# Kernel optimization log

Measured on AMD Instinct MI355X. Metric: run time of the kernel, lower is better.

Reference implementation:

```python
import jax, jax.numpy as jnp
import numpy as np

D_MODEL = 1024
N_HEADS = 16
D_K = D_MODEL // N_HEADS
D_FF = 4096
EPS = 1e-5


def _layer_norm(x, gamma, beta):
    mu = jnp.mean(x, axis=-1, keepdims=True)
    var = jnp.var(x, axis=-1, keepdims=True)
    return (x - mu) * jax.lax.rsqrt(var + EPS) * gamma + beta


def setup_inputs() -> dict:
    key = jax.random.key(0)
    ks = jax.random.split(key, 16)
    s = 1.0 / np.sqrt(D_MODEL)
    sf = 1.0 / np.sqrt(D_FF)
    return {
        "x": jax.random.normal(ks[0], (2, 2048, D_MODEL), dtype=jnp.float32),
        "Wq": jax.random.uniform(ks[1], (D_MODEL, D_MODEL), minval=-s, maxval=s),
        "bq": jax.random.uniform(ks[2], (D_MODEL,), minval=-s, maxval=s),
        "Wk": jax.random.uniform(ks[3], (D_MODEL, D_MODEL), minval=-s, maxval=s),
        "bk": jax.random.uniform(ks[4], (D_MODEL,), minval=-s, maxval=s),
        "Wv": jax.random.uniform(ks[5], (D_MODEL, D_MODEL), minval=-s, maxval=s),
        "bv": jax.random.uniform(ks[6], (D_MODEL,), minval=-s, maxval=s),
        "Wo": jax.random.uniform(ks[7], (D_MODEL, D_MODEL), minval=-s, maxval=s),
        "bo": jax.random.uniform(ks[8], (D_MODEL,), minval=-s, maxval=s),
        "W1": jax.random.uniform(ks[9], (D_MODEL, D_FF), minval=-s, maxval=s),
        "b1": jax.random.uniform(ks[10], (D_FF,), minval=-s, maxval=s),
        "W2": jax.random.uniform(ks[11], (D_FF, D_MODEL), minval=-sf, maxval=sf),
        "b2": jax.random.uniform(ks[12], (D_MODEL,), minval=-sf, maxval=sf),
        "g1": jnp.ones((D_MODEL,)),
        "be1": jnp.zeros((D_MODEL,)),
        "g2": jnp.ones((D_MODEL,)),
        "be2": jnp.zeros((D_MODEL,)),
    }


def reference(x, Wq, bq, Wk, bk, Wv, bv, Wo, bo, W1, b1, W2, b2, g1, be1, g2, be2):
    B, S, _ = x.shape

    def heads(y):  # (B,S,D) -> (B,H,S,dk)
        return y.reshape(B, S, N_HEADS, D_K).transpose(0, 2, 1, 3)

    q = heads(x @ Wq + bq)
    k = heads(x @ Wk + bk)
    v = heads(x @ Wv + bv)

    scores = jnp.einsum("bhqd,bhkd->bhqk", q, k) / np.sqrt(D_K)
    attn = jax.nn.softmax(scores, axis=-1)
    out = jnp.einsum("bhqk,bhkd->bhqd", attn, v)
    out = out.transpose(0, 2, 1, 3).reshape(B, S, D_MODEL)
    attn_out = out @ Wo + bo

    resid_mid = _layer_norm(x + attn_out, g1, be1)
    ff = jnp.maximum(resid_mid @ W1 + b1, 0.0) @ W2 + b2
    return _layer_norm(resid_mid + ff, g2, be2)
```

## Files before the change

kernel.cpp:

```cpp
#include <hip/hip_runtime.h>

#define DM   1024
#define DFF  4096
#define NH   16
#define DKH  64
#define SEQ  2048
#define BATCH 2
#define ROWS (BATCH*SEQ)
#define QKS  2048

typedef __bf16 bf16x8 __attribute__((ext_vector_type(8)));
typedef float  f32x4  __attribute__((ext_vector_type(4)));

__device__ __forceinline__ unsigned short f2b(float f) {
    unsigned int u = __builtin_bit_cast(unsigned int, f);
    u += 0x7fffu + ((u >> 16) & 1u);
    return (unsigned short)(u >> 16);
}
__device__ __forceinline__ float b2f(unsigned short u) {
    return __builtin_bit_cast(float, (unsigned int)u << 16);
}
__device__ __forceinline__ float exp2_raw(float x) {
    float r;
    asm("v_exp_f32 %0, %1" : "=v"(r) : "v"(x));
    return r;
}

__device__ __forceinline__ void gl_lds16(const unsigned short* g, unsigned short* l) {
    __builtin_amdgcn_global_load_lds(
        (const __attribute__((address_space(1))) unsigned int*)(const void*)g,
        (__attribute__((address_space(3))) unsigned int*)(void*)l, 16, 0, 0);
}

__global__ __launch_bounds__(256) void k_prep(const float* __restrict__ x,
                                              const float* __restrict__ Wq,
                                              const float* __restrict__ Wk,
                                              const float* __restrict__ Wv,
                                              const float* __restrict__ Wo,
                                              const float* __restrict__ W1,
                                              const float* __restrict__ W2,
                                              unsigned short* __restrict__ xb,
                                              unsigned short* __restrict__ WqkT,
                                              unsigned short* __restrict__ WvT,
                                              unsigned short* __restrict__ WoT,
                                              unsigned short* __restrict__ W1T,
                                              unsigned short* __restrict__ W2T) {
    int z = blockIdx.z;
    int bid = blockIdx.y * gridDim.x + blockIdx.x;
    int tx = threadIdx.x, ty = threadIdx.y;
    if (z == 6) {
        int i = bid * 256 + ty * 32 + tx;
        float4 v = ((const float4*)x)[i];
        ushort4 u;
        u.x = f2b(v.x); u.y = f2b(v.y); u.z = f2b(v.z); u.w = f2b(v.w);
        ((ushort4*)xb)[i] = u;
        return;
    }
    const float* W; unsigned short* WT; int R, C;
    if      (z == 0) { W = Wq; WT = WqkT;                     R = DM;  C = DM;  }
    else if (z == 1) { W = Wk; WT = WqkT + (size_t)DM * DM;   R = DM;  C = DM;  }
    else if (z == 2) { W = Wv; WT = WvT;                      R = DM;  C = DM;  }
    else if (z == 3) { W = Wo; WT = WoT;                      R = DM;  C = DM;  }
    else if (z == 4) { W = W1; WT = W1T;                      R = DM;  C = DFF; }
    else             { W = W2; WT = W2T;                      R = DFF; C = DM;  }
    int ct = C / 32;
    if (bid >= (R / 32) * ct) return;
    int c0 = (bid % ct) * 32, r0 = (bid / ct) * 32;
    __shared__ float t[32][33];
#pragma unroll
    for (int i = 0; i < 4; i++) {
        int r = ty + i * 8;
        t[r][tx] = W[(size_t)(r0 + r) * C + c0 + tx];
    }
    __syncthreads();
#pragma unroll
    for (int i = 0; i < 4; i++) {
        int r = ty + i * 8;
        WT[(size_t)(c0 + r) * R + r0 + tx] = f2b(t[tx][r]);
    }
}

template<int WM, int WN, bool OUTF32, bool RELU, bool BIASROW, bool VPERM, bool SCALE2, bool SPLITK, bool SUPER2D>
__global__ __launch_bounds__(256) void k_gemm_bt(const unsigned short* __restrict__ A,
                                                 const unsigned short* __restrict__ BT,
                                                 const float* __restrict__ bias,
                                                 const float* __restrict__ bias2,
                                                 int bsplit, float sc2,
                                                 void* __restrict__ Cout,
                                                 int M, int N, int K) {
    constexpr int BM = 2 * WM, BN = 2 * WN;
    constexpr int MT = WM / 16, NT = WN / 16;
    constexpr int IA = BM / 32, IB = BN / 32;
    __shared__ unsigned short As[BM][64] __attribute__((aligned(16)));
    __shared__ unsigned short Bs[BN][64] __attribute__((aligned(16)));
    int tid = threadIdx.x;
    int w = tid >> 6, l = tid & 63;
    int wr = w >> 1, wc = w & 1;
    int l15 = l & 15, lg = l >> 4;

    int bid = blockIdx.y * gridDim.x + blockIdx.x;
    int nwg = gridDim.x * gridDim.y;
    int m0, n0;
    if (SUPER2D) {
        int xcd = bid & 7, q = bid >> 3;
        int RM = gridDim.y >> 1, RN = gridDim.x >> 2;
        int mI = (xcd >> 2) * RM + (q % RM);
        int nI = (xcd & 3) * RN + (q / RM);
        m0 = mI * BM; n0 = nI * BN;
    } else {
        int swz = (bid & 7) * (nwg >> 3) + (bid >> 3);
        m0 = (swz / gridDim.x) * BM; n0 = (swz % gridDim.x) * BN;
    }

    int kb_ = SPLITK ? (int)blockIdx.z * (K >> 1) : 0;
    int Keff = SPLITK ? (K >> 1) : K;

    int lr8 = l >> 3;
    int gsrc = (l & 7) ^ lr8;
    const unsigned short* Abase = A  + (size_t)(m0 + w * (BM / 4) + lr8) * K + kb_ + gsrc * 8;
    const unsigned short* Bbase = BT + (size_t)(n0 + w * (BN / 4) + lr8) * K + kb_ + gsrc * 8;

    f32x4 acc[MT][NT] = {};

    int nk = Keff >> 6;
    for (int kt = 0; kt < nk; ++kt) {
        __syncthreads();
#pragma unroll
        for (int it = 0; it < IA; ++it)
            gl_lds16(Abase + (size_t)(it * 8) * K + kt * 64, &As[w * (BM / 4) + it * 8][0]);
#pragma unroll
        for (int it = 0; it < IB; ++it)
            gl_lds16(Bbase + (size_t)(it * 8) * K + kt * 64, &Bs[w * (BN / 4) + it * 8][0]);
        __syncthreads();
#pragma unroll
        for (int ks = 0; ks < 2; ++ks) {
            int glog = ks * 4 + lg;
            bf16x8 af[MT], bfr[NT];
#pragma unroll
            for (int mt = 0; mt < MT; ++mt) {
                int row = wr * WM + mt * 16 + l15;
                af[mt] = *(const bf16x8*)&As[row][(glog ^ (row & 7)) << 3];
            }
#pragma unroll
            for (int nt = 0; nt < NT; ++nt) {
                int row = wc * WN + nt * 16 + l15;
                bfr[nt] = *(const bf16x8*)&Bs[row][(glog ^ (row & 7)) << 3];
            }
#pragma unroll
            for (int mt = 0; mt < MT; ++mt)
#pragma unroll
                for (int nt = 0; nt < NT; ++nt)
                    acc[mt][nt] = __builtin_amdgcn_mfma_f32_16x16x32_bf16(af[mt], bfr[nt], acc[mt][nt], 0, 0, 0);
        }
    }
    float*          CoutF = (float*)Cout          + (SPLITK ? (size_t)blockIdx.z * M * N : 0);
    unsigned short* CoutH = (unsigned short*)Cout + (SPLITK ? (size_t)blockIdx.z * M * N : 0);
    float browv[MT][4];
    if (BIASROW) {
#pragma unroll
        for (int mt = 0; mt < MT; ++mt)
#pragma unroll
            for (int r = 0; r < 4; ++r)
                browv[mt][r] = bias[m0 + wr * WM + mt * 16 + lg * 4 + r];
    }
#pragma unroll
    for (int nt = 0; nt < NT; ++nt) {
        int colo = VPERM ? (32 * (nt >> 1) + 4 * (nt & 1) + 8 * (l15 >> 2) + (l15 & 3))
                         : (nt * 16 + l15);
        int col = n0 + wc * WN + colo;
        float bv = BIASROW ? 0.f : (col < bsplit ? bias[col] : bias2[col - bsplit]);
        if (SPLITK && blockIdx.z != 0) bv = 0.f;
#pragma unroll
        for (int mt = 0; mt < MT; ++mt) {
#pragma unroll
            for (int r = 0; r < 4; ++r) {
                int row = m0 + wr * WM + mt * 16 + lg * 4 + r;
                float v = acc[mt][nt][r] + (BIASROW ? browv[mt][r] : bv);
                if (SCALE2 && col >= bsplit) v *= sc2;
                if (RELU) v = fmaxf(v, 0.f);
                if (OUTF32) CoutF[(size_t)row * N + col] = v;
                else        CoutH[(size_t)row * N + col] = f2b(v);
            }
        }
    }
}

__global__ __launch_bounds__(256) void k_gemm_qkv(const unsigned short* __restrict__ xb,
                                                  const unsigned short* __restrict__ WqkT,
                                                  const unsigned short* __restrict__ WvT,
                                                  const float* __restrict__ bq,
                                                  const float* __restrict__ bk,
                                                  const float* __restrict__ bv,
                                                  float sc,
                                                  unsigned short* __restrict__ qkb,
                                                  unsigned short* __restrict__ vT) {
    constexpr int BM = 64, BN = 128, MT = 2, NT = 4, IA = 2, IB = 4;
    const int K = DM;
    __shared__ unsigned short As[BM][64] __attribute__((aligned(16)));
    __shared__ unsigned short Bs[BN][64] __attribute__((aligned(16)));
    int tid = threadIdx.x;
    int w = tid >> 6, l = tid & 63;
    int wr = w >> 1, wc = w & 1;
    int l15 = l & 15, lg = l >> 4;

    int bid1 = blockIdx.x;
    bool isQK = bid1 < 1024;
    const unsigned short *A, *BT;
    int m0, n0;
    if (isQK) {
        int bid = bid1;
        int swz = (bid & 7) * 128 + (bid >> 3);
        m0 = (swz / 16) * BM; n0 = (swz % 16) * BN;
        A = xb; BT = WqkT;
    } else {
        int bid = bid1 - 1024;
        int swz = (bid & 7) * 64 + (bid >> 3);
        m0 = (swz / 32) * BM; n0 = (swz % 32) * BN;
        A = WvT; BT = xb;
    }

    int lr8 = l >> 3;
    int gsrc = (l & 7) ^ lr8;
    const unsigned short* Abase = A  + (size_t)(m0 + w * (BM / 4) + lr8) * K + gsrc * 8;
    const unsigned short* Bbase = BT + (size_t)(n0 + w * (BN / 4) + lr8) * K + gsrc * 8;

    f32x4 acc[MT][NT] = {};

    for (int kt = 0; kt < K / 64; ++kt) {
        __syncthreads();
#pragma unroll
        for (int it = 0; it < IA; ++it)
            gl_lds16(Abase + (size_t)(it * 8) * K + kt * 64, &As[w * (BM / 4) + it * 8][0]);
#pragma unroll
        for (int it = 0; it < IB; ++it)
            gl_lds16(Bbase + (size_t)(it * 8) * K + kt * 64, &Bs[w * (BN / 4) + it * 8][0]);
        __syncthreads();
#pragma unroll
        for (int ks = 0; ks < 2; ++ks) {
            int glog = ks * 4 + lg;
            bf16x8 af[MT], bfr[NT];
#pragma unroll
            for (int mt = 0; mt < MT; ++mt) {
                int row = wr * 32 + mt * 16 + l15;
                af[mt] = *(const bf16x8*)&As[row][(glog ^ (row & 7)) << 3];
            }
#pragma unroll
            for (int nt = 0; nt < NT; ++nt) {
                int row = wc * 64 + nt * 16 + l15;
                bfr[nt] = *(const bf16x8*)&Bs[row][(glog ^ (row & 7)) << 3];
            }
#pragma unroll
            for (int mt = 0; mt < MT; ++mt)
#pragma unroll
                for (int nt = 0; nt < NT; ++nt)
                    acc[mt][nt] = __builtin_amdgcn_mfma_f32_16x16x32_bf16(af[mt], bfr[nt], acc[mt][nt], 0, 0, 0);
        }
    }

    if (isQK) {
#pragma unroll
        for (int nt = 0; nt < NT; ++nt) {
            int col = n0 + wc * 64 + nt * 16 + l15;
            float bvx = col < DM ? bq[col] : bk[col - DM];
#pragma unroll
            for (int mt = 0; mt < MT; ++mt)
#pragma unroll
                for (int r = 0; r < 4; ++r) {
                    int row = m0 + wr * 32 + mt * 16 + lg * 4 + r;
                    float v = acc[mt][nt][r] + bvx;
                    if (col >= DM) v *= sc;
                    qkb[(size_t)row * QKS + col] = f2b(v);
                }
        }
    } else {
        float browv[MT][4];
#pragma unroll
        for (int mt = 0; mt < MT; ++mt)
#pragma unroll
            for (int r = 0; r < 4; ++r)
                browv[mt][r] = bv[m0 + wr * 32 + mt * 16 + lg * 4 + r];
#pragma unroll
        for (int nt = 0; nt < NT; ++nt) {
            int colo = 32 * (nt >> 1) + 4 * (nt & 1) + 8 * (l15 >> 2) + (l15 & 3);
            int col = n0 + wc * 64 + colo;
#pragma unroll
            for (int mt = 0; mt < MT; ++mt)
#pragma unroll
                for (int r = 0; r < 4; ++r) {
                    int row = m0 + wr * 32 + mt * 16 + lg * 4 + r;
                    vT[(size_t)row * ROWS + col] = f2b(acc[mt][nt][r] + browv[mt][r]);
                }
        }
    }
}

__global__ __launch_bounds__(512) void k_attn(const unsigned short* __restrict__ Q,
                                              const unsigned short* __restrict__ Kb,
                                              const unsigned short* __restrict__ VT,
                                              unsigned short* __restrict__ O) {
    __shared__ unsigned short ks[2][128][64] __attribute__((aligned(16)));
    __shared__ unsigned short vs[2][2][64][64] __attribute__((aligned(16)));

    int tid = threadIdx.x;
    int w = tid >> 6, l = tid & 63;
    int l15 = l & 15, lg = l >> 4;

    int bid = blockIdx.y * gridDim.x + blockIdx.x;
    int bh = (bid & 7) * 4 + ((bid >> 3) & 3);
    int qt = bid >> 5;
    int b = bh >> 4, h = bh & 15;
    int row0 = qt * 128;

    const unsigned short* qg  = Q  + (size_t)b * SEQ * QKS + h * DKH;
    const unsigned short* kg  = Kb + (size_t)b * SEQ * QKS + h * DKH;
    const unsigned short* vtg = VT + (size_t)(h * DKH) * ROWS + (size_t)b * SEQ;

    int lr8 = l >> 3;
    int gsrc = (l & 7) ^ lr8;

    const unsigned short* kp = kg  + (size_t)(w * 16 + lr8) * QKS + gsrc * 8;
    const unsigned short* vp = vtg + (size_t)(w * 8 + lr8) * ROWS + gsrc * 8;

    gl_lds16(kp,                  &ks[0][w * 16][0]);
    gl_lds16(kp + (size_t)8 * QKS, &ks[0][w * 16 + 8][0]);
    gl_lds16(vp,                  &vs[0][0][w * 8][0]);
    gl_lds16(vp + 64,             &vs[0][1][w * 8][0]);
    kp += (size_t)128 * QKS; vp += 128;

    bf16x8 aq[2];
    {
        int qrow = row0 + w * 16 + l15;
        aq[0] = *(const bf16x8*)(qg + (size_t)qrow * QKS + lg * 8);
        aq[1] = *(const bf16x8*)(qg + (size_t)qrow * QKS + (4 + lg) * 8);
    }

    int dsoff[2][4];
#pragma unroll
    for (int ksi = 0; ksi < 2; ksi++)
#pragma unroll
        for (int nt = 0; nt < 4; nt++) {
            int row = nt * 16 + l15;
            int glog = ksi * 4 + lg;
            dsoff[ksi][nt] = row * 128 + ((glog ^ (row & 7)) << 4);
        }

    union { bf16x8 v; unsigned int u[4]; } ones;
#pragma unroll
    for (int i = 0; i < 4; i++) ones.u[i] = 0x3f803f80u;

    f32x4 o[4] = {};
    f32x4 osum = {};

    __syncthreads();

    int cur = 0;
    for (int kt = 0; kt < SEQ / 128; ++kt) {
        if (kt + 1 < SEQ / 128) {
            gl_lds16(kp,                   &ks[cur ^ 1][w * 16][0]);
            gl_lds16(kp + (size_t)8 * QKS, &ks[cur ^ 1][w * 16 + 8][0]);
            gl_lds16(vp,                   &vs[cur ^ 1][0][w * 8][0]);
            gl_lds16(vp + 64,              &vs[cur ^ 1][1][w * 8][0]);
            kp += (size_t)128 * QKS; vp += 128;
        }

#pragma unroll
        for (int hf = 0; hf < 2; ++hf) {
            const char* kbase = (const char*)&ks[cur][hf * 64][0];
            const char* vbase = (const char*)&vs[cur][hf][0][0];

            f32x4 s[4] = {};
            __builtin_amdgcn_s_setprio(1);
#pragma unroll
            for (int ksi = 0; ksi < 2; ksi++)
#pragma unroll
                for (int nt = 0; nt < 4; nt++) {
                    bf16x8 bk = *(const bf16x8*)(kbase + dsoff[ksi][nt]);
                    s[nt] = __builtin_amdgcn_mfma_f32_16x16x32_bf16(bk, aq[ksi], s[nt], 0, 0, 0);
                }
            __builtin_amdgcn_s_setprio(0);

            union { bf16x8 v; unsigned int u[4]; } A0, A1;
#pragma unroll
            for (int nt = 0; nt < 4; nt++)
#pragma unroll
                for (int w2 = 0; w2 < 2; w2++) {
                    float e0 = exp2_raw(s[nt][2 * w2]);
                    float e1 = exp2_raw(s[nt][2 * w2 + 1]);
                    unsigned int pk;
                    asm("v_cvt_pk_bf16_f32 %0, %1, %2" : "=v"(pk) : "v"(e0), "v"(e1));
                    if (nt < 2) A0.u[(nt & 1) * 2 + w2] = pk;
                    else        A1.u[(nt & 1) * 2 + w2] = pk;
                }

            __builtin_amdgcn_s_setprio(1);
            osum = __builtin_amdgcn_mfma_f32_16x16x32_bf16(A0.v, ones.v, osum, 0, 0, 0);
            osum = __builtin_amdgcn_mfma_f32_16x16x32_bf16(A1.v, ones.v, osum, 0, 0, 0);
#pragma unroll
            for (int ksi = 0; ksi < 2; ksi++)
#pragma unroll
                for (int nt = 0; nt < 4; nt++) {
                    bf16x8 bv = *(const bf16x8*)(vbase + dsoff[ksi][nt]);
                    o[nt] = __builtin_amdgcn_mfma_f32_16x16x32_bf16(ksi == 0 ? A0.v : A1.v, bv, o[nt], 0, 0, 0);
                }
            __builtin_amdgcn_s_setprio(0);
        }

        __syncthreads();
        cur ^= 1;
    }

    float rinv[4];
#pragma unroll
    for (int r = 0; r < 4; r++) rinv[r] = 1.f / osum[r];

    unsigned short* og = O + (size_t)b * SEQ * DM + h * DKH;
#pragma unroll
    for (int nt = 0; nt < 4; nt++) {
        int d = nt * 16 + l15;
#pragma unroll
        for (int r = 0; r < 4; r++) {
            int srow_ = row0 + w * 16 + lg * 4 + r;
            og[(size_t)srow_ * DM + d] = f2b(o[nt][r] * rinv[r]);
        }
    }
}

template<bool A16, bool WF32, bool WB16, bool ADD3, bool BC16>
__global__ __launch_bounds__(256) void k_add_ln(const void* __restrict__ a,
                                                const void* __restrict__ b,
                                                const void* __restrict__ c,
                                                const float* __restrict__ gamma,
                                                const float* __restrict__ beta,
                                                float* __restrict__ outf,
                                                unsigned short* __restrict__ outb) {
    __shared__ float red[8];
    int row = blockIdx.x, tid = threadIdx.x;
    float4 va;
    if (A16) {
        ushort4 ua = ((const ushort4*)((const unsigned short*)a + (size_t)row * DM))[tid];
        va.x = b2f(ua.x); va.y = b2f(ua.y); va.z = b2f(ua.z); va.w = b2f(ua.w);
    } else {
        va = ((const float4*)((const float*)a + (size_t)row * DM))[tid];
    }
    float4 vb, vc;
    if (BC16) {
        ushort4 ub = ((const ushort4*)((const unsigned short*)b + (size_t)row * DM))[tid];
        vb.x = b2f(ub.x); vb.y = b2f(ub.y); vb.z = b2f(ub.z); vb.w = b2f(ub.w);
    } else {
        vb = ((const float4*)((const float*)b + (size_t)row * DM))[tid];
    }
    float4 v;
    v.x = va.x + vb.x; v.y = va.y + vb.y; v.z = va.z + vb.z; v.w = va.w + vb.w;
    if (ADD3) {
        if (BC16) {
            ushort4 uc = ((const ushort4*)((const unsigned short*)c + (size_t)row * DM))[tid];
            vc.x = b2f(uc.x); vc.y = b2f(uc.y); vc.z = b2f(uc.z); vc.w = b2f(uc.w);
        } else {
            vc = ((const float4*)((const float*)c + (size_t)row * DM))[tid];
        }
        v.x += vc.x; v.y += vc.y; v.z += vc.z; v.w += vc.w;
    }
    float s = v.x + v.y + v.z + v.w;
    float q = v.x * v.x + v.y * v.y + v.z * v.z + v.w * v.w;
#pragma unroll
    for (int m = 1; m < 64; m <<= 1) { s += __shfl_xor(s, m); q += __shfl_xor(q, m); }
    if ((tid & 63) == 0) { red[tid >> 6] = s; red[4 + (tid >> 6)] = q; }
    __syncthreads();
    float tot  = red[0] + red[1] + red[2] + red[3];
    float totq = red[4] + red[5] + red[6] + red[7];
    float mu = tot * (1.f / DM);
    float var = totq * (1.f / DM) - mu * mu;
    float rs = rsqrtf(var + 1e-5f);
    float4 g  = ((const float4*)gamma)[tid];
    float4 be = ((const float4*)beta)[tid];
    float4 y;
    y.x = (v.x - mu) * rs * g.x + be.x;
    y.y = (v.y - mu) * rs * g.y + be.y;
    y.z = (v.z - mu) * rs * g.z + be.z;
    y.w = (v.w - mu) * rs * g.w + be.w;
    if (WF32) ((float4*)(outf + (size_t)row * DM))[tid] = y;
    if (WB16) {
        ushort4 u;
        u.x = f2b(y.x); u.y = f2b(y.y); u.z = f2b(y.z); u.w = f2b(y.w);
        ((ushort4*)(outb + (size_t)row * DM))[tid] = u;
    }
}

extern "C" void kernel_launch(void* const* d_in, const int* in_sizes, int n_in,
                              void* d_out, int out_size, void* d_ws, size_t ws_size,
                              hipStream_t stream) {
    const float* x   = (const float*)d_in[0];
    const float* Wq  = (const float*)d_in[1];
    const float* bq  = (const float*)d_in[2];
    const float* Wk  = (const float*)d_in[3];
    const float* bk  = (const float*)d_in[4];
    const float* Wv  = (const float*)d_in[5];
    const float* bv  = (const float*)d_in[6];
    const float* Wo  = (const float*)d_in[7];
    const float* bo  = (const float*)d_in[8];
    const float* W1  = (const float*)d_in[9];
    const float* b1  = (const float*)d_in[10];
    const float* W2  = (const float*)d_in[11];
    const float* b2  = (const float*)d_in[12];
    const float* g1  = (const float*)d_in[13];
    const float* be1 = (const float*)d_in[14];
    const float* g2  = (const float*)d_in[15];
    const float* be2 = (const float*)d_in[16];

    char* ws = (char*)d_ws;
    const size_t MB = 1u << 20;
    unsigned short* xb    = (unsigned short*)(ws + 0);
    unsigned short* WqkT  = (unsigned short*)(ws + 8 * MB);
    unsigned short* WvT   = (unsigned short*)(ws + 12 * MB);
    unsigned short* WoT   = (unsigned short*)(ws + 14 * MB);
    unsigned short* W1T   = (unsigned short*)(ws + 16 * MB);
    unsigned short* W2T   = (unsigned short*)(ws + 24 * MB);
    unsigned short* qkb   = (unsigned short*)(ws + 32 * MB);
    unsigned short* vT    = (unsigned short*)(ws + 48 * MB);
    unsigned short* prtb  = (unsigned short*)(ws + 32 * MB);
    unsigned short* residb= (unsigned short*)(ws + 88 * MB);
    unsigned short* h1    = (unsigned short*)(ws + 96 * MB);

    dim3 blk(256);
    const int BIG = 1 << 30;
    const float SC = 0.125f * 1.44269504f;

    k_prep<<<dim3(128, 32, 7), dim3(32, 8), 0, stream>>>(x, Wq, Wk, Wv, Wo, W1, W2,
                                                         xb, WqkT, WvT, WoT, W1T, W2T);

    k_gemm_qkv<<<dim3(1536), blk, 0, stream>>>(xb, WqkT, WvT, bq, bk, bv, SC, qkb, vT);

    k_attn<<<dim3(SEQ / 128, BATCH * NH), dim3(512), 0, stream>>>(qkb, qkb + DM, vT, xb);

    k_gemm_bt<32, 64, false, false, false, false, false, true, false><<<dim3(DM / 128, ROWS / 64, 2), blk, 0, stream>>>(
        xb, WoT, bo, bo, BIG, 1.f, prtb, ROWS, DM, DM);
    k_add_ln<false, false, true, true, true><<<ROWS, blk, 0, stream>>>(
        x, prtb, prtb + (size_t)ROWS * DM, g1, be1, nullptr, residb);

    k_gemm_bt<64, 64, false, true, false, false, false, false, true><<<dim3(DFF / 128, ROWS / 128), blk, 0, stream>>>(
        residb, W1T, b1, b1, BIG, 1.f, h1, ROWS, DFF, DM);
    k_gemm_bt<32, 64, false, false, false, false, false, true, false><<<dim3(DM / 128, ROWS / 64, 2), blk, 0, stream>>>(
        h1, W2T, b2, b2, BIG, 1.f, prtb, ROWS, DM, DFF);
    k_add_ln<true, true, false, true, true><<<ROWS, blk, 0, stream>>>(
        residb, prtb, prtb + (size_t)ROWS * DM, g2, be2, (float*)d_out, nullptr);
}
```

Measured before the change: 217.2 us.

## Split attention KV sequence across two wave groups and combine partials in LDS

The attention kernel now launches 1024 threads per block. Two groups of 8 waves each process half of the key/value sequence (1024 keys) for the same 128 query rows, using 64-key tiles with per-group double buffers. At the end, group 1 writes its unnormalized output and row sums to LDS, and group 0 adds them before normalizing and storing. The aim is more waves in flight per query tile to hide latency, at the cost of an extra barrier, an LDS reduction and higher register pressure from launch_bounds(1024, 8). This only works because the softmax uses no running max, so partial sums can be added directly.

```diff
diff --git a/kernel.cpp b/kernel.cpp
--- a/kernel.cpp
+++ b/kernel.cpp
@@ -294,15 +294,15 @@
     }
 }
 
-__global__ __launch_bounds__(512) void k_attn(const unsigned short* __restrict__ Q,
-                                              const unsigned short* __restrict__ Kb,
-                                              const unsigned short* __restrict__ VT,
-                                              unsigned short* __restrict__ O) {
-    __shared__ unsigned short ks[2][128][64] __attribute__((aligned(16)));
-    __shared__ unsigned short vs[2][2][64][64] __attribute__((aligned(16)));
+__global__ __launch_bounds__(1024, 8) void k_attn(const unsigned short* __restrict__ Q,
+                                                  const unsigned short* __restrict__ Kb,
+                                                  const unsigned short* __restrict__ VT,
+                                                  unsigned short* __restrict__ O) {
+    __shared__ unsigned short lds[32768] __attribute__((aligned(16)));
 
     int tid = threadIdx.x;
     int w = tid >> 6, l = tid & 63;
+    int wg = w >> 3, wl = w & 7;
     int l15 = l & 15, lg = l >> 4;
 
     int bid = blockIdx.y * gridDim.x + blockIdx.x;
@@ -318,18 +318,20 @@
     int lr8 = l >> 3;
     int gsrc = (l & 7) ^ lr8;
 
-    const unsigned short* kp = kg  + (size_t)(w * 16 + lr8) * QKS + gsrc * 8;
-    const unsigned short* vp = vtg + (size_t)(w * 8 + lr8) * ROWS + gsrc * 8;
-
-    gl_lds16(kp,                  &ks[0][w * 16][0]);
-    gl_lds16(kp + (size_t)8 * QKS, &ks[0][w * 16 + 8][0]);
-    gl_lds16(vp,                  &vs[0][0][w * 8][0]);
-    gl_lds16(vp + 64,             &vs[0][1][w * 8][0]);
-    kp += (size_t)128 * QKS; vp += 128;
+    unsigned short* kbuf[2] = { lds + (wg * 2 + 0) * 4096, lds + (wg * 2 + 1) * 4096 };
+    unsigned short* vbuf[2] = { lds + 16384 + (wg * 2 + 0) * 4096,
+                                lds + 16384 + (wg * 2 + 1) * 4096 };
+
+    const unsigned short* kp = kg  + (size_t)(wg * 1024 + wl * 8 + lr8) * QKS + gsrc * 8;
+    const unsigned short* vp = vtg + (size_t)(wl * 8 + lr8) * ROWS + wg * 1024 + gsrc * 8;
+
+    gl_lds16(kp, kbuf[0] + (wl * 8) * 64);
+    gl_lds16(vp, vbuf[0] + (wl * 8) * 64);
+    kp += (size_t)64 * QKS; vp += 64;
 
     bf16x8 aq[2];
     {
-        int qrow = row0 + w * 16 + l15;
+        int qrow = row0 + wl * 16 + l15;
         aq[0] = *(const bf16x8*)(qg + (size_t)qrow * QKS + lg * 8);
         aq[1] = *(const bf16x8*)(qg + (size_t)qrow * QKS + (4 + lg) * 8);
     }
@@ -354,73 +356,89 @@
     __syncthreads();
 
     int cur = 0;
-    for (int kt = 0; kt < SEQ / 128; ++kt) {
-        if (kt + 1 < SEQ / 128) {
-            gl_lds16(kp,                   &ks[cur ^ 1][w * 16][0]);
-            gl_lds16(kp + (size_t)8 * QKS, &ks[cur ^ 1][w * 16 + 8][0]);
-            gl_lds16(vp,                   &vs[cur ^ 1][0][w * 8][0]);
-            gl_lds16(vp + 64,              &vs[cur ^ 1][1][w * 8][0]);
-            kp += (size_t)128 * QKS; vp += 128;
-        }
-
-#pragma unroll
-        for (int hf = 0; hf < 2; ++hf) {
-            const char* kbase = (const char*)&ks[cur][hf * 64][0];
-            const char* vbase = (const char*)&vs[cur][hf][0][0];
-
-            f32x4 s[4] = {};
-            __builtin_amdgcn_s_setprio(1);
-#pragma unroll
-            for (int ksi = 0; ksi < 2; ksi++)
-#pragma unroll
-                for (int nt = 0; nt < 4; nt++) {
-                    bf16x8 bk = *(const bf16x8*)(kbase + dsoff[ksi][nt]);
-                    s[nt] = __builtin_amdgcn_mfma_f32_16x16x32_bf16(bk, aq[ksi], s[nt], 0, 0, 0);
-                }
-            __builtin_amdgcn_s_setprio(0);
-
-            union { bf16x8 v; unsigned int u[4]; } A0, A1;
-#pragma unroll
-            for (int nt = 0; nt < 4; nt++)
-#pragma unroll
-                for (int w2 = 0; w2 < 2; w2++) {
-                    float e0 = exp2_raw(s[nt][2 * w2]);
-                    float e1 = exp2_raw(s[nt][2 * w2 + 1]);
-                    unsigned int pk;
-                    asm("v_cvt_pk_bf16_f32 %0, %1, %2" : "=v"(pk) : "v"(e0), "v"(e1));
-                    if (nt < 2) A0.u[(nt & 1) * 2 + w2] = pk;
-                    else        A1.u[(nt & 1) * 2 + w2] = pk;
-                }
-
-            __builtin_amdgcn_s_setprio(1);
-            osum = __builtin_amdgcn_mfma_f32_16x16x32_bf16(A0.v, ones.v, osum, 0, 0, 0);
-            osum = __builtin_amdgcn_mfma_f32_16x16x32_bf16(A1.v, ones.v, osum, 0, 0, 0);
-#pragma unroll
-            for (int ksi = 0; ksi < 2; ksi++)
-#pragma unroll
-                for (int nt = 0; nt < 4; nt++) {
-                    bf16x8 bv = *(const bf16x8*)(vbase + dsoff[ksi][nt]);
-                    o[nt] = __builtin_amdgcn_mfma_f32_16x16x32_bf16(ksi == 0 ? A0.v : A1.v, bv, o[nt], 0, 0, 0);
-                }
-            __builtin_amdgcn_s_setprio(0);
-        }
+    for (int kt = 0; kt < 16; ++kt) {
+        if (kt + 1 < 16) {
+            gl_lds16(kp, kbuf[cur ^ 1] + (wl * 8) * 64);
+            gl_lds16(vp, vbuf[cur ^ 1] + (wl * 8) * 64);
+            kp += (size_t)64 * QKS; vp += 64;
+        }
+
+        const char* kbase = (const char*)kbuf[cur];
+        const char* vbase = (const char*)vbuf[cur];
+
+        f32x4 s[4] = {};
+        __builtin_amdgcn_s_setprio(1);
+#pragma unroll
+        for (int ksi = 0; ksi < 2; ksi++)
+#pragma unroll
+            for (int nt = 0; nt < 4; nt++) {
+                bf16x8 bk = *(const bf16x8*)(kbase + dsoff[ksi][nt]);
+                s[nt] = __builtin_amdgcn_mfma_f32_16x16x32_bf16(bk, aq[ksi], s[nt], 0, 0, 0);
+            }
+        __builtin_amdgcn_s_setprio(0);
+
+        union { bf16x8 v; unsigned int u[4]; } A0, A1;
+#pragma unroll
+        for (int nt = 0; nt < 4; nt++)
+#pragma unroll
+            for (int w2 = 0; w2 < 2; w2++) {
+                float e0 = exp2_raw(s[nt][2 * w2]);
+                float e1 = exp2_raw(s[nt][2 * w2 + 1]);
+                unsigned int pk;
+                asm("v_cvt_pk_bf16_f32 %0, %1, %2" : "=v"(pk) : "v"(e0), "v"(e1));
+                if (nt < 2) A0.u[(nt & 1) * 2 + w2] = pk;
+                else        A1.u[(nt & 1) * 2 + w2] = pk;
+            }
+
+        __builtin_amdgcn_s_setprio(1);
+        osum = __builtin_amdgcn_mfma_f32_16x16x32_bf16(A0.v, ones.v, osum, 0, 0, 0);
+        osum = __builtin_amdgcn_mfma_f32_16x16x32_bf16(A1.v, ones.v, osum, 0, 0, 0);
+#pragma unroll
+        for (int ksi = 0; ksi < 2; ksi++)
+#pragma unroll
+            for (int nt = 0; nt < 4; nt++) {
+                bf16x8 bv = *(const bf16x8*)(vbase + dsoff[ksi][nt]);
+                o[nt] = __builtin_amdgcn_mfma_f32_16x16x32_bf16(ksi == 0 ? A0.v : A1.v, bv, o[nt], 0, 0, 0);
+            }
+        __builtin_amdgcn_s_setprio(0);
 
         __syncthreads();
         cur ^= 1;
     }
 
-    float rinv[4];
-#pragma unroll
-    for (int r = 0; r < 4; r++) rinv[r] = 1.f / osum[r];
-
-    unsigned short* og = O + (size_t)b * SEQ * DM + h * DKH;
-#pragma unroll
-    for (int nt = 0; nt < 4; nt++) {
-        int d = nt * 16 + l15;
-#pragma unroll
-        for (int r = 0; r < 4; r++) {
-            int srow_ = row0 + w * 16 + lg * 4 + r;
-            og[(size_t)srow_ * DM + d] = f2b(o[nt][r] * rinv[r]);
+    float* comb = (float*)lds;
+    if (wg == 1) {
+        float* p = comb + (size_t)(wl * 64 + l) * 20;
+#pragma unroll
+        for (int nt = 0; nt < 4; nt++)
+#pragma unroll
+            for (int r = 0; r < 4; r++) p[nt * 4 + r] = o[nt][r];
+#pragma unroll
+        for (int r = 0; r < 4; r++) p[16 + r] = osum[r];
+    }
+    __syncthreads();
+    if (wg == 0) {
+        float* p = comb + (size_t)(wl * 64 + l) * 20;
+#pragma unroll
+        for (int nt = 0; nt < 4; nt++)
+#pragma unroll
+            for (int r = 0; r < 4; r++) o[nt][r] += p[nt * 4 + r];
+#pragma unroll
+        for (int r = 0; r < 4; r++) osum[r] += p[16 + r];
+
+        float rinv[4];
+#pragma unroll
+        for (int r = 0; r < 4; r++) rinv[r] = 1.f / osum[r];
+
+        unsigned short* og = O + (size_t)b * SEQ * DM + h * DKH;
+#pragma unroll
+        for (int nt = 0; nt < 4; nt++) {
+            int d = nt * 16 + l15;
+#pragma unroll
+            for (int r = 0; r < 4; r++) {
+                int srow_ = row0 + wl * 16 + lg * 4 + r;
+                og[(size_t)srow_ * DM + d] = f2b(o[nt][r] * rinv[r]);
+            }
         }
     }
 }
@@ -530,7 +548,7 @@
 
     k_gemm_qkv<<<dim3(1536), blk, 0, stream>>>(xb, WqkT, WvT, bq, bk, bv, SC, qkb, vT);
 
-    k_attn<<<dim3(SEQ / 128, BATCH * NH), dim3(512), 0, stream>>>(qkb, qkb + DM, vT, xb);
+    k_attn<<<dim3(SEQ / 128, BATCH * NH), dim3(1024), 0, stream>>>(qkb, qkb + DM, vT, xb);
 
     k_gemm_bt<32, 64, false, false, false, false, false, true, false><<<dim3(DM / 128, ROWS / 64, 2), blk, 0, stream>>>(
         xb, WoT, bo, bo, BIG, 1.f, prtb, ROWS, DM, DM);
```

Result: no change. 216.4 us (-0.4%).
